# Optimization experiments

Measured on AMD Instinct MI355X. Metric: run time of the kernel, lower is better.

## Reference

```python
import jax, jax.numpy as jnp
import numpy as np

N_NODES = 100000
N_EDGES = 1600000
F_IN = 64
F_HID = 64


def setup_inputs() -> dict:
    key = jax.random.key(0)
    k = jax.random.split(key, 6)
    x = jax.random.normal(k[0], (N_NODES, F_IN), dtype=jnp.float32)
    edge_src = jax.random.randint(k[1], (N_EDGES,), 0, N_NODES, dtype=jnp.int32)
    edge_dst = jax.random.randint(k[2], (N_EDGES,), 0, N_NODES, dtype=jnp.int32)
    W1 = jax.random.normal(k[3], (2 * F_IN, F_HID), dtype=jnp.float32) * 0.05
    b1 = jnp.zeros((F_HID,), dtype=jnp.float32)
    W2 = jax.random.normal(k[4], (2 * F_HID, F_HID), dtype=jnp.float32) * 0.05
    b2 = jnp.zeros((F_HID,), dtype=jnp.float32)
    return {"x": x, "edge_src": edge_src, "edge_dst": edge_dst,
            "W1": W1, "b1": b1, "W2": W2, "b2": b2}


def _mean_aggregate(x, edge_src, edge_dst):
    # gather neighbor features along edges, segment-mean into destination nodes
    msgs = x[edge_src]                                            # [E, F]
    summed = jax.ops.segment_sum(msgs, edge_dst, num_segments=N_NODES)  # [N, F]
    cnt = jax.ops.segment_sum(jnp.ones_like(edge_dst, dtype=x.dtype),
                              edge_dst, num_segments=N_NODES)      # [N]
    # nodes with no neighbors -> zero vector (matches torch loop behavior)
    return summed / jnp.maximum(cnt, 1.0)[:, None]


def _sage_layer(x, edge_src, edge_dst, W, b):
    neigh_mean = _mean_aggregate(x, edge_src, edge_dst)
    h = jnp.concatenate([x, neigh_mean], axis=1)                  # [N, 2F]
    return jax.nn.relu(h @ W + b)


def reference(x, edge_src, edge_dst, W1, b1, W2, b2):
    h = _sage_layer(x, edge_src, edge_dst, W1, b1)
    h = _sage_layer(h, edge_src, edge_dst, W2, b2)
    return h
```

## Files before the change

kernel.cpp:

```cpp
#include <hip/hip_runtime.h>
#include <hip/hip_bf16.h>


constexpr int N_NODES = 100000;
constexpr int N_EDGES = 1600000;
constexpr int F = 64;
constexpr int NBK = 64;
constexpr int NBK_USED = (N_NODES + 2047) / 2048;
constexpr int PART_T = 512;
constexpr int PART_E = 4096;
constexpr int PART_BLOCKS = (N_EDGES + PART_E - 1) / PART_E;
constexpr int COUNT_BLOCKS = (N_EDGES + 2047) / 2048;
constexpr int LDW = 136;

typedef short short8 __attribute__((ext_vector_type(8)));
typedef float floatx4 __attribute__((ext_vector_type(4)));

__device__ __forceinline__ float bf2f(ushort u) {
    union { unsigned int i; float f; } c; c.i = (unsigned int)u << 16; return c.f;
}
__device__ __forceinline__ ushort f2bf(float v) {
    union { float f; unsigned int i; } c; c.f = v;
    unsigned int r = c.i + 0x7fffu + ((c.i >> 16) & 1u);
    return (ushort)(r >> 16);
}


__global__ void __launch_bounds__(256)
count_kernel(const int* __restrict__ edst, int* __restrict__ bcnt) {
    __shared__ int lb[NBK];
    int t = threadIdx.x;
    if (t < NBK) lb[t] = 0;
    __syncthreads();
    int base = blockIdx.x * 2048;
    #pragma unroll
    for (int k = 0; k < 8; ++k) {
        int e = base + k * 256 + t;
        if (e < N_EDGES) atomicAdd(&lb[edst[e] >> 11], 1);
    }
    __syncthreads();
    if (t < NBK && lb[t]) atomicAdd(&bcnt[t], lb[t]);
}

__global__ void __launch_bounds__(64)
scan_b64_kernel(const int* __restrict__ bcnt, int* __restrict__ bbase,
                int* __restrict__ bcur, int* __restrict__ rp) {
    if (threadIdx.x == 0) {
        int run = 0;
        for (int i = 0; i < NBK; ++i) {
            bbase[i] = run; bcur[i] = run; run += bcnt[i];
        }
        rp[N_NODES] = run;
    }
}

__global__ void __launch_bounds__(PART_T)
part_kernel(const int* __restrict__ esrc, const int* __restrict__ edst,
            int* __restrict__ bcur, int2* __restrict__ ebuf) {
    __shared__ int cnt[NBK];
    __shared__ int lbase[NBK];
    __shared__ int gbase[NBK];
    __shared__ int2 stage[PART_E];
    int t = threadIdx.x;
    if (t < NBK) cnt[t] = 0;
    __syncthreads();
    int base = blockIdx.x * PART_E;
    int2 ed[8]; int bk[8]; int rk[8];
    #pragma unroll
    for (int k = 0; k < 8; ++k) {
        int e = base + k * PART_T + t;
        if (e < N_EDGES) {
            ed[k].x = esrc[e];
            ed[k].y = edst[e];
            bk[k] = ed[k].y >> 11;
            rk[k] = atomicAdd(&cnt[bk[k]], 1);
        } else {
            bk[k] = -1; rk[k] = 0; ed[k] = make_int2(0, 0);
        }
    }
    __syncthreads();
    if (t == 0) {
        int run = 0;
        for (int i = 0; i < NBK; ++i) { lbase[i] = run; run += cnt[i]; }
    }
    __syncthreads();
    if (t < NBK) gbase[t] = cnt[t] ? atomicAdd(&bcur[t], cnt[t]) : 0;
    __syncthreads();
    #pragma unroll
    for (int k = 0; k < 8; ++k)
        if (bk[k] >= 0) stage[lbase[bk[k]] + rk[k]] = ed[k];
    __syncthreads();
    for (int b = 0; b < NBK; ++b) {
        int len = cnt[b], l0 = lbase[b], g0 = gbase[b];
        for (int i = t; i < len; i += PART_T) ebuf[g0 + i] = stage[l0 + i];
    }
}

__global__ void __launch_bounds__(1024)
csr_bucket_kernel(const int2* __restrict__ ebuf, const int* __restrict__ bbase,
                  const int* __restrict__ bcnt,
                  int* __restrict__ rp, int* __restrict__ ss) {
    __shared__ int sdeg[2048];
    __shared__ int spart[1024];
    int b = blockIdx.x;
    int lo = b << 11;
    int nn = N_NODES - lo; if (nn > 2048) nn = 2048;
    int bstart = bbase[b];
    int bn = bcnt[b];
    int t = threadIdx.x;

    sdeg[t] = 0; sdeg[t + 1024] = 0;
    __syncthreads();
    for (int i = t; i < bn; i += 1024)
        atomicAdd(&sdeg[ebuf[bstart + i].y - lo], 1);
    __syncthreads();

    int a0 = sdeg[2 * t], a1 = sdeg[2 * t + 1];
    spart[t] = a0 + a1;
    __syncthreads();
    for (int off = 1; off < 1024; off <<= 1) {
        int v = spart[t];
        int add = (t >= off) ? spart[t - off] : 0;
        __syncthreads();
        spart[t] = v + add;
        __syncthreads();
    }
    int ex = (t == 0) ? 0 : spart[t - 1];
    sdeg[2 * t]     = ex;
    sdeg[2 * t + 1] = ex + a0;
    if (2 * t < nn)     rp[lo + 2 * t]     = bstart + ex;
    if (2 * t + 1 < nn) rp[lo + 2 * t + 1] = bstart + ex + a0;
    __syncthreads();

    for (int i = t; i < bn; i += 1024) {
        int2 p = ebuf[bstart + i];
        int pos = atomicAdd(&sdeg[p.y - lo], 1);
        ss[bstart + pos] = p.x;
    }
}

__global__ void __launch_bounds__(256)
conv_kernel(const float* __restrict__ x, ushort* __restrict__ xh) {
    int i = blockIdx.x * 256 + threadIdx.x;
    float4 v = ((const float4*)x)[i];
    ushort4 o;
    o.x = f2bf(v.x); o.y = f2bf(v.y); o.z = f2bf(v.z); o.w = f2bf(v.w);
    ((ushort4*)xh)[i] = o;
}

__global__ void __launch_bounds__(512)
prep_w_kernel(const float* __restrict__ W1, const float* __restrict__ W2,
              ushort* __restrict__ Wt1, ushort* __restrict__ Wt2) {
    const float* W = blockIdx.x ? W2 : W1;
    ushort* Wt = blockIdx.x ? Wt2 : Wt1;
    for (int i = threadIdx.x; i < 2 * F * F; i += 512) {
        int k = i >> 6, f = i & 63;
        Wt[f * LDW + k] = f2bf(W[i]);
    }
}

__global__ void __launch_bounds__(512)
fused_sage_kernel(const ushort* __restrict__ xh,
                  const int* __restrict__ rp,
                  const int* __restrict__ ss,
                  const ushort* __restrict__ Wt,
                  const float* __restrict__ bias,
                  ushort* __restrict__ out_bf,
                  float* __restrict__ out_f)
{
    __shared__ ushort sWt[F * LDW];
    __shared__ ushort cin[32 * LDW];

    {
        const int* src = (const int*)Wt;
        int* dst = (int*)sWt;
        for (int i = threadIdx.x; i < F * LDW / 2; i += 512) dst[i] = src[i];
    }

    const int w    = threadIdx.x >> 6;
    const int lane = threadIdx.x & 63;
    const int half = lane >> 5;
    const int p    = lane & 31;

    const unsigned int* __restrict__ xw = (const unsigned int*)xh;

    for (int q = 0; q < 4; ++q) {
        const int n = blockIdx.x * 32 + w * 4 + q;
        int start = rp[n];
        int end   = rp[n + 1];
        float ax = 0.0f, ay = 0.0f;

        int i = start;
        for (; i + 8 <= end; i += 8) {
            int e0 = i + half;
            int s0 = ss[e0], s1 = ss[e0 + 2], s2 = ss[e0 + 4], s3 = ss[e0 + 6];
            unsigned int u0 = xw[(size_t)s0 * 32 + p];
            unsigned int u1 = xw[(size_t)s1 * 32 + p];
            unsigned int u2 = xw[(size_t)s2 * 32 + p];
            unsigned int u3 = xw[(size_t)s3 * 32 + p];
            ax += bf2f((ushort)u0) + bf2f((ushort)u1)
                + bf2f((ushort)u2) + bf2f((ushort)u3);
            ay += bf2f((ushort)(u0 >> 16)) + bf2f((ushort)(u1 >> 16))
                + bf2f((ushort)(u2 >> 16)) + bf2f((ushort)(u3 >> 16));
        }
        for (; i + 2 <= end; i += 2) {
            int s0 = ss[i + half];
            unsigned int u0 = xw[(size_t)s0 * 32 + p];
            ax += bf2f((ushort)u0);
            ay += bf2f((ushort)(u0 >> 16));
        }
        if (i < end && half == 0) {
            int s0 = ss[i];
            unsigned int u0 = xw[(size_t)s0 * 32 + p];
            ax += bf2f((ushort)u0);
            ay += bf2f((ushort)(u0 >> 16));
        }
        ax += __shfl_xor(ax, 32);
        ay += __shfl_xor(ay, 32);

        if (half == 0) {
            unsigned int* crow = (unsigned int*)&cin[(w * 4 + q) * LDW];
            crow[p] = xw[(size_t)n * 32 + p];
            float scale = 1.0f / fmaxf((float)(end - start), 1.0f);
            unsigned int lo = f2bf(ax * scale);
            unsigned int hi = f2bf(ay * scale);
            crow[32 + p] = (hi << 16) | lo;
        }
    }
    __syncthreads();

    const int Mt = w >> 2, Nt = w & 3;
    const int r16 = lane & 15, g4 = lane >> 4;
    floatx4 acc = {0.0f, 0.0f, 0.0f, 0.0f};
    #pragma unroll
    for (int ks = 0; ks < 4; ++ks) {
        short8 a = *(const short8*)&cin[(Mt * 16 + r16) * LDW + ks * 32 + g4 * 8];
        short8 b = *(const short8*)&sWt[(Nt * 16 + r16) * LDW + ks * 32 + g4 * 8];
        acc = __builtin_amdgcn_mfma_f32_16x16x32_bf16(a, b, acc, 0, 0, 0);
    }
    const int feat = Nt * 16 + r16;
    const float bv = bias[feat];
    #pragma unroll
    for (int reg = 0; reg < 4; ++reg) {
        int node = blockIdx.x * 32 + Mt * 16 + g4 * 4 + reg;
        float r = fmaxf(acc[reg] + bv, 0.0f);
        if (out_bf) out_bf[(size_t)node * F + feat] = f2bf(r);
        if (out_f)  out_f [(size_t)node * F + feat] = r;
    }
}

extern "C" void kernel_launch(void* const* d_in, const int* in_sizes, int n_in,
                              void* d_out, int out_size, void* d_ws, size_t ws_size,
                              hipStream_t stream) {
    const float* x    = (const float*)d_in[0];
    const int*   esrc = (const int*)d_in[1];
    const int*   edst = (const int*)d_in[2];
    const float* W1   = (const float*)d_in[3];
    const float* b1   = (const float*)d_in[4];
    const float* W2   = (const float*)d_in[5];
    const float* b2   = (const float*)d_in[6];
    float* out = (float*)d_out;

    int*    bcnt   = (int*)d_ws;
    int*    bbase  = bcnt + NBK;
    int*    bcur   = bbase + NBK;
    int*    rp     = bcur + NBK + 64;
    int*    ss     = rp + (N_NODES + 12);
    ushort* xh     = (ushort*)(ss + N_EDGES);
    ushort* h1h    = xh + (size_t)N_NODES * F;
    int2*   ebuf   = (int2*)h1h;
    ushort* Wt1g   = h1h + (size_t)N_NODES * F;
    ushort* Wt2g   = Wt1g + F * LDW;

    const int NB = N_NODES / 32;
    const int CB = (N_NODES * F / 4) / 256;

    hipMemsetAsync(bcnt, 0, NBK * 4, stream);
    count_kernel<<<COUNT_BLOCKS, 256, 0, stream>>>(edst, bcnt);
    scan_b64_kernel<<<1, 64, 0, stream>>>(bcnt, bbase, bcur, rp);
    part_kernel<<<PART_BLOCKS, PART_T, 0, stream>>>(esrc, edst, bcur, ebuf);
    csr_bucket_kernel<<<NBK_USED, 1024, 0, stream>>>(ebuf, bbase, bcnt, rp, ss);
    conv_kernel<<<CB, 256, 0, stream>>>(x, xh);
    prep_w_kernel<<<2, 512, 0, stream>>>(W1, W2, Wt1g, Wt2g);

    fused_sage_kernel<<<NB, 512, 0, stream>>>(xh,  rp, ss, Wt1g, b1, h1h, nullptr);
    fused_sage_kernel<<<NB, 512, 0, stream>>>(h1h, rp, ss, Wt2g, b2, nullptr, out);
}
```

Measured before the change: 327.7 us.

## Use finer 512-node CSR buckets and merge weight prep into scan kernel

Shrinks the destination buckets from 2048 to 512 nodes, giving 196 CSR-build blocks instead of 49 so more CUs work on the bucketed CSR construction. The partition kernel now uses a parallel prefix scan over the 256 bucket counts, and its copy-out is split across waves, each handling 32 buckets. The weight transpose/convert is folded into the scan kernel to drop one launch. In exchange, each partition block writes more, smaller scattered segments, and the serial single-thread scan runs over 256 entries.

New measurement: 303.5 us. 1.08x faster.

```diff
diff --git a/kernel.cpp b/kernel.cpp
--- a/kernel.cpp
+++ b/kernel.cpp
@@ -5,8 +5,10 @@
 constexpr int N_NODES = 100000;
 constexpr int N_EDGES = 1600000;
 constexpr int F = 64;
-constexpr int NBK = 64;
-constexpr int NBK_USED = (N_NODES + 2047) / 2048;
+constexpr int SH = 9;
+constexpr int SPAN = 1 << SH;
+constexpr int NBK = 256;
+constexpr int NBK_USED = (N_NODES + SPAN - 1) / SPAN;
 constexpr int PART_T = 512;
 constexpr int PART_E = 4096;
 constexpr int PART_BLOCKS = (N_EDGES + PART_E - 1) / PART_E;
@@ -30,27 +32,38 @@
 count_kernel(const int* __restrict__ edst, int* __restrict__ bcnt) {
     __shared__ int lb[NBK];
     int t = threadIdx.x;
-    if (t < NBK) lb[t] = 0;
+    lb[t] = 0;
     __syncthreads();
     int base = blockIdx.x * 2048;
     #pragma unroll
     for (int k = 0; k < 8; ++k) {
         int e = base + k * 256 + t;
-        if (e < N_EDGES) atomicAdd(&lb[edst[e] >> 11], 1);
-    }
-    __syncthreads();
-    if (t < NBK && lb[t]) atomicAdd(&bcnt[t], lb[t]);
-}
-
-__global__ void __launch_bounds__(64)
-scan_b64_kernel(const int* __restrict__ bcnt, int* __restrict__ bbase,
-                int* __restrict__ bcur, int* __restrict__ rp) {
-    if (threadIdx.x == 0) {
+        if (e < N_EDGES) atomicAdd(&lb[edst[e] >> SH], 1);
+    }
+    __syncthreads();
+    if (lb[t]) atomicAdd(&bcnt[t], lb[t]);
+}
+
+__global__ void __launch_bounds__(512)
+scan_prep_kernel(const int* __restrict__ bcnt, int* __restrict__ bbase,
+                 int* __restrict__ bcur, int* __restrict__ rp,
+                 const float* __restrict__ W1, const float* __restrict__ W2,
+                 ushort* __restrict__ Wt1, ushort* __restrict__ Wt2) {
+    __shared__ int sb[NBK];
+    int t = threadIdx.x;
+    if (t < NBK) sb[t] = bcnt[t];
+    __syncthreads();
+    if (t == 0) {
         int run = 0;
-        for (int i = 0; i < NBK; ++i) {
-            bbase[i] = run; bcur[i] = run; run += bcnt[i];
-        }
+        for (int i = 0; i < NBK; ++i) { int v = sb[i]; sb[i] = run; run += v; }
         rp[N_NODES] = run;
+    }
+    __syncthreads();
+    if (t < NBK) { bbase[t] = sb[t]; bcur[t] = sb[t]; }
+    for (int i = t; i < 2 * F * F; i += 512) {
+        int k = i >> 6, f = i & 63;
+        Wt1[f * LDW + k] = f2bf(W1[i]);
+        Wt2[f * LDW + k] = f2bf(W2[i]);
     }
 }
 
@@ -72,16 +85,25 @@
         if (e < N_EDGES) {
             ed[k].x = esrc[e];
             ed[k].y = edst[e];
-            bk[k] = ed[k].y >> 11;
+            bk[k] = ed[k].y >> SH;
             rk[k] = atomicAdd(&cnt[bk[k]], 1);
         } else {
             bk[k] = -1; rk[k] = 0; ed[k] = make_int2(0, 0);
         }
     }
     __syncthreads();
-    if (t == 0) {
-        int run = 0;
-        for (int i = 0; i < NBK; ++i) { lbase[i] = run; run += cnt[i]; }
+    {
+        int v = 0;
+        if (t < NBK) { v = cnt[t]; lbase[t] = v; }
+        __syncthreads();
+        for (int off = 1; off < NBK; off <<= 1) {
+            int add = 0;
+            if (t < NBK && t >= off) add = lbase[t - off];
+            __syncthreads();
+            if (t < NBK) lbase[t] += add;
+            __syncthreads();
+        }
+        if (t < NBK) lbase[t] -= v;
     }
     __syncthreads();
     if (t < NBK) gbase[t] = cnt[t] ? atomicAdd(&bcur[t], cnt[t]) : 0;
@@ -90,49 +112,49 @@
     for (int k = 0; k < 8; ++k)
         if (bk[k] >= 0) stage[lbase[bk[k]] + rk[k]] = ed[k];
     __syncthreads();
-    for (int b = 0; b < NBK; ++b) {
-        int len = cnt[b], l0 = lbase[b], g0 = gbase[b];
-        for (int i = t; i < len; i += PART_T) ebuf[g0 + i] = stage[l0 + i];
-    }
-}
-
-__global__ void __launch_bounds__(1024)
+    {
+        int w = t >> 6, lane = t & 63;
+        for (int b = w * 32; b < w * 32 + 32; ++b) {
+            int len = cnt[b], l0 = lbase[b], g0 = gbase[b];
+            for (int i = lane; i < len; i += 64) ebuf[g0 + i] = stage[l0 + i];
+        }
+    }
+}
+
+__global__ void __launch_bounds__(512)
 csr_bucket_kernel(const int2* __restrict__ ebuf, const int* __restrict__ bbase,
                   const int* __restrict__ bcnt,
                   int* __restrict__ rp, int* __restrict__ ss) {
-    __shared__ int sdeg[2048];
-    __shared__ int spart[1024];
+    __shared__ int sdeg[SPAN];
+    __shared__ int sc[SPAN];
     int b = blockIdx.x;
-    int lo = b << 11;
-    int nn = N_NODES - lo; if (nn > 2048) nn = 2048;
+    int lo = b << SH;
     int bstart = bbase[b];
     int bn = bcnt[b];
     int t = threadIdx.x;
 
-    sdeg[t] = 0; sdeg[t + 1024] = 0;
-    __syncthreads();
-    for (int i = t; i < bn; i += 1024)
+    sdeg[t] = 0;
+    __syncthreads();
+    for (int i = t; i < bn; i += 512)
         atomicAdd(&sdeg[ebuf[bstart + i].y - lo], 1);
     __syncthreads();
 
-    int a0 = sdeg[2 * t], a1 = sdeg[2 * t + 1];
-    spart[t] = a0 + a1;
-    __syncthreads();
-    for (int off = 1; off < 1024; off <<= 1) {
-        int v = spart[t];
-        int add = (t >= off) ? spart[t - off] : 0;
+    int a = sdeg[t];
+    sc[t] = a;
+    __syncthreads();
+    for (int off = 1; off < SPAN; off <<= 1) {
+        int v = sc[t];
+        int add = (t >= off) ? sc[t - off] : 0;
         __syncthreads();
-        spart[t] = v + add;
+        sc[t] = v + add;
         __syncthreads();
     }
-    int ex = (t == 0) ? 0 : spart[t - 1];
-    sdeg[2 * t]     = ex;
-    sdeg[2 * t + 1] = ex + a0;
-    if (2 * t < nn)     rp[lo + 2 * t]     = bstart + ex;
-    if (2 * t + 1 < nn) rp[lo + 2 * t + 1] = bstart + ex + a0;
-    __syncthreads();
-
-    for (int i = t; i < bn; i += 1024) {
+    int ex = sc[t] - a;
+    sdeg[t] = ex;
+    if (lo + t < N_NODES) rp[lo + t] = bstart + ex;
+    __syncthreads();
+
+    for (int i = t; i < bn; i += 512) {
         int2 p = ebuf[bstart + i];
         int pos = atomicAdd(&sdeg[p.y - lo], 1);
         ss[bstart + pos] = p.x;
@@ -146,17 +168,6 @@
     ushort4 o;
     o.x = f2bf(v.x); o.y = f2bf(v.y); o.z = f2bf(v.z); o.w = f2bf(v.w);
     ((ushort4*)xh)[i] = o;
-}
-
-__global__ void __launch_bounds__(512)
-prep_w_kernel(const float* __restrict__ W1, const float* __restrict__ W2,
-              ushort* __restrict__ Wt1, ushort* __restrict__ Wt2) {
-    const float* W = blockIdx.x ? W2 : W1;
-    ushort* Wt = blockIdx.x ? Wt2 : Wt1;
-    for (int i = threadIdx.x; i < 2 * F * F; i += 512) {
-        int k = i >> 6, f = i & 63;
-        Wt[f * LDW + k] = f2bf(W[i]);
-    }
 }
 
 __global__ void __launch_bounds__(512)
@@ -264,8 +275,8 @@
     int*    bcnt   = (int*)d_ws;
     int*    bbase  = bcnt + NBK;
     int*    bcur   = bbase + NBK;
-    int*    rp     = bcur + NBK + 64;
-    int*    ss     = rp + (N_NODES + 12);
+    int*    rp     = bcur + NBK;
+    int*    ss     = rp + (N_NODES + 8);
     ushort* xh     = (ushort*)(ss + N_EDGES);
     ushort* h1h    = xh + (size_t)N_NODES * F;
     int2*   ebuf   = (int2*)h1h;
@@ -277,11 +288,11 @@
 
     hipMemsetAsync(bcnt, 0, NBK * 4, stream);
     count_kernel<<<COUNT_BLOCKS, 256, 0, stream>>>(edst, bcnt);
-    scan_b64_kernel<<<1, 64, 0, stream>>>(bcnt, bbase, bcur, rp);
+    scan_prep_kernel<<<1, 512, 0, stream>>>(bcnt, bbase, bcur, rp,
+                                            W1, W2, Wt1g, Wt2g);
     part_kernel<<<PART_BLOCKS, PART_T, 0, stream>>>(esrc, edst, bcur, ebuf);
-    csr_bucket_kernel<<<NBK_USED, 1024, 0, stream>>>(ebuf, bbase, bcnt, rp, ss);
+    csr_bucket_kernel<<<NBK_USED, 512, 0, stream>>>(ebuf, bbase, bcnt, rp, ss);
     conv_kernel<<<CB, 256, 0, stream>>>(x, xh);
-    prep_w_kernel<<<2, 512, 0, stream>>>(W1, W2, Wt1g, Wt2g);
 
     fused_sage_kernel<<<NB, 512, 0, stream>>>(xh,  rp, ss, Wt1g, b1, h1h, nullptr);
     fused_sage_kernel<<<NB, 512, 0, stream>>>(h1h, rp, ss, Wt2g, b2, nullptr, out);
```
